# Kernel tuning notes

Hardware: AMD Instinct MI355X
Metric: run time of the kernel (lower is better)

Reference implementation:

```python
import jax, jax.numpy as jnp
import numpy as np

B, S, D, H = 2, 2048, 1024, 16
DEPTH = D // H


def setup_inputs() -> dict:
    key = jax.random.key(0)
    ks = jax.random.split(key, 12)
    sc = 1.0 / np.sqrt(D)
    n = lambda k, shp, s=sc: jax.random.normal(k, shp, dtype=jnp.float32) * s
    return {
        "q": jax.random.normal(ks[0], (B, S, D), dtype=jnp.float32),
        "k": jax.random.normal(ks[1], (B, S, D), dtype=jnp.float32),
        "v": jax.random.normal(ks[2], (B, S, D), dtype=jnp.float32),
        # key-padding mask: 1 = masked, 0 = keep (added to logits * -1e9)
        "mask": (jax.random.uniform(ks[3], (B, 1, 1, S)) < 0.1).astype(jnp.float32),
        "wq_w": n(ks[4], (D, D)), "wq_b": jnp.zeros((D,), jnp.float32),
        "wk_w": n(ks[5], (D, D)), "wk_b": jnp.zeros((D,), jnp.float32),
        "wv_w": n(ks[6], (D, D)), "wv_b": jnp.zeros((D,), jnp.float32),
        "dense_w": n(ks[7], (D, D)), "dense_b": jnp.zeros((D,), jnp.float32),
    }


def _split_heads(x, b, s):
    # [B, S, D] -> [B, H, S, depth]
    return x.reshape(b, s, H, DEPTH).transpose(0, 2, 1, 3)


def reference(q, k, v, mask, wq_w, wq_b, wk_w, wk_b, wv_w, wv_b, dense_w, dense_b):
    b, sq, _ = q.shape
    sk = k.shape[1]
    qh = _split_heads(q @ wq_w.T + wq_b, b, sq)
    kh = _split_heads(k @ wk_w.T + wk_b, b, sk)
    vh = _split_heads(v @ wv_w.T + wv_b, b, sk)
    scale = 1.0 / jnp.sqrt(jnp.float32(DEPTH))
    logits = jnp.einsum('bhqd,bhkd->bhqk', qh, kh) * scale  # [B,H,Sq,Sk]
    logits = logits + mask * (-1e9)
    attn = jax.nn.softmax(logits, axis=-1)
    ctx = jnp.einsum('bhqk,bhkd->bhqd', attn, vh)
    ctx = ctx.transpose(0, 2, 1, 3).reshape(b, sq, D)  # concat heads
    out = ctx @ dense_w.T + dense_b
    return out, attn
```

## Files before the change

kernel.cpp:

```cpp
#include <hip/hip_runtime.h>

#define BB 2
#define SS 2048
#define DD 1024
#define HH 16
#define DEPTH 64
#define MTOT (BB*SS)
#define QW 8
#define QBLK (QW*16)
#define NT (SS/64)
#define NPROJ ((size_t)BB*HH*SS*DEPTH)
#define WSZ   ((size_t)DD*DD)

using f16 = _Float16;
typedef _Float16 f16x8 __attribute__((ext_vector_type(8)));
typedef _Float16 f16x4 __attribute__((ext_vector_type(4)));
typedef float f32x4 __attribute__((ext_vector_type(4)));

#define GLOAD16(g, l) __builtin_amdgcn_global_load_lds(                      \
    (__attribute__((address_space(1))) const void*)(g),                      \
    (__attribute__((address_space(3))) void*)(l), 16, 0, 0)

__global__ __launch_bounds__(256) void cvt_kernel(
    const float* __restrict__ q, const float* __restrict__ k, const float* __restrict__ v,
    const float* __restrict__ w0, const float* __restrict__ w1, const float* __restrict__ w2,
    f16* __restrict__ qf, f16* __restrict__ kf, f16* __restrict__ vf,
    f16* __restrict__ wq, f16* __restrict__ wk, f16* __restrict__ wv)
{
    const int z = blockIdx.y;
    const float* s = z==0?q : z==1?k : z==2?v : z==3?w0 : z==4?w1 : w2;
    f16*        d = z==0?qf: z==1?kf: z==2?vf: z==3?wq: z==4?wk: wv;
    const size_t n = (z < 3) ? NPROJ : WSZ;
    for (size_t i = ((size_t)blockIdx.x * 256 + threadIdx.x) * 8; i < n;
         i += (size_t)gridDim.x * 256 * 8) {
        f32x4 a = *(const f32x4*)(s + i);
        f32x4 b = *(const f32x4*)(s + i + 4);
        f16x8 o = {(f16)a[0], (f16)a[1], (f16)a[2], (f16)a[3],
                   (f16)b[0], (f16)b[1], (f16)b[2], (f16)b[3]};
        *(f16x8*)(d + i) = o;
    }
}

__global__ __launch_bounds__(256) void proj_kernel(
    const f16* __restrict__ qf, const f16* __restrict__ kf, const f16* __restrict__ vf,
    const f16* __restrict__ wqw, const f16* __restrict__ wkw, const f16* __restrict__ wvw,
    const float* __restrict__ bq, const float* __restrict__ bk, const float* __restrict__ bv,
    f16* __restrict__ qh, f16* __restrict__ kh, f16* __restrict__ vt)
{
    const int mode = blockIdx.z;
    const f16* A    = mode==0 ? qf  : mode==1 ? kf  : vf;
    const f16* Bw   = mode==0 ? wqw : mode==1 ? wkw : wvw;
    const float* bias = mode==0 ? bq : mode==1 ? bk : bv;

    __shared__ f16 As[128*64];
    __shared__ f16 Bs[128*64];

    const int tid = threadIdx.x, wave = tid >> 6, lane = tid & 63;
    const int m0 = blockIdx.y * 128, n0 = blockIdx.x * 128;
    const int wm = (wave >> 1) * 64, wn = (wave & 1) * 64;
    const int lrow = lane & 15, g = lane >> 4;
    const int sw = lrow & 7;
    const int srow = tid >> 3;
    const int schk = (tid & 7) ^ (srow & 7);

    f32x4 acc[4][4] = {};

    for (int kk = 0; kk < DD; kk += 64) {
        #pragma unroll
        for (int i = 0; i < 4; ++i) {
            GLOAD16(A  + (size_t)(m0 + i*32 + srow) * DD + kk + schk * 8,
                    &As[i*2048 + wave*512]);
            GLOAD16(Bw + (size_t)(n0 + i*32 + srow) * DD + kk + schk * 8,
                    &Bs[i*2048 + wave*512]);
        }
        __syncthreads();
        for (int kf2 = 0; kf2 < 2; ++kf2) {
            f16x8 a[4], bf[4];
            for (int i = 0; i < 4; ++i)
                a[i]  = *(const f16x8*)&As[(wm + i*16 + lrow)*64 + ((kf2*4 + g) ^ sw)*8];
            for (int i = 0; i < 4; ++i)
                bf[i] = *(const f16x8*)&Bs[(wn + i*16 + lrow)*64 + ((kf2*4 + g) ^ sw)*8];
            for (int mi = 0; mi < 4; ++mi)
                for (int ni = 0; ni < 4; ++ni)
                    acc[mi][ni] = __builtin_amdgcn_mfma_f32_16x16x32_f16(a[mi], bf[ni], acc[mi][ni], 0, 0, 0);
        }
        __syncthreads();
    }

    const int rbase = g * 4;
    if (mode == 2) {
        for (int ni = 0; ni < 4; ++ni) {
            int n = n0 + wn + ni * 16 + lrow;
            float bval = bias[n];
            int hh = n >> 6, dep = n & 63;
            for (int mi = 0; mi < 4; ++mi) {
                int m = m0 + wm + mi * 16 + rbase;
                int bb = m >> 11, s = m & 2047;
                f16x4 pk = {(f16)(acc[mi][ni][0] + bval), (f16)(acc[mi][ni][1] + bval),
                            (f16)(acc[mi][ni][2] + bval), (f16)(acc[mi][ni][3] + bval)};
                *(f16x4*)&vt[((size_t)(bb * HH + hh) * DEPTH + dep) * SS + s] = pk;
            }
        }
    } else {
        f16* dst = (mode == 0) ? qh : kh;
        for (int ni = 0; ni < 4; ++ni) {
            int n = n0 + wn + ni * 16 + lrow;
            float bval = bias[n];
            int hh = n >> 6, dep = n & 63;
            for (int mi = 0; mi < 4; ++mi)
                for (int j = 0; j < 4; ++j) {
                    int m = m0 + wm + mi * 16 + rbase + j;
                    int bb = m >> 11, s = m & 2047;
                    dst[((size_t)(bb * HH + hh) * SS + s) * DEPTH + dep] = (f16)(acc[mi][ni][j] + bval);
                }
        }
    }
}

__global__ __launch_bounds__(512) void attn_kernel(
    const f16* __restrict__ qh, const f16* __restrict__ kh, const f16* __restrict__ vt,
    const float* __restrict__ mask, float* __restrict__ attn_out, f16* __restrict__ ctx)
{
    __shared__ float mlds[SS];
    __shared__ f16 Ks[2][64*64];
    __shared__ f16 Vs[2][64*64];
    __shared__ f16 Pl[QW][16][72];

    const int tid = threadIdx.x, wave = tid >> 6, lane = tid & 63;
    const int L = blockIdx.x;
    const int xcd = L & 7, iw = L >> 3;
    const int bh = xcd * 4 + (iw >> 4);
    const int qb = iw & 15;
    const int b = bh >> 4, h = bh & 15;
    const int q0 = qb * QBLK;
    const int lrow = lane & 15, g = lane >> 4;
    const int rbase = g * 4;
    const int sw = lrow & 7;
    const int srow = tid >> 3;
    const int schk = (tid & 7) ^ (srow & 7);

    const f16* Qbase = qh + (size_t)bh * SS * DEPTH;
    const f16* Kb = kh + (size_t)bh * SS * DEPTH;
    const f16* Vb = vt + (size_t)bh * DEPTH * SS;

    for (int i = tid; i < SS; i += 512) mlds[i] = mask[b * SS + i] * -1e9f;

    f16x8 aq[2];
    for (int kf2 = 0; kf2 < 2; ++kf2)
        aq[kf2] = *(const f16x8*)(Qbase + (size_t)(q0 + wave*16 + lrow) * DEPTH + kf2*32 + g*8);

    float s_l[4] = {0.f, 0.f, 0.f, 0.f};
    GLOAD16(Kb + (size_t)(0*64 + srow) * DEPTH + schk * 8, &Ks[0][wave * 512]);
    __syncthreads();
    for (int kt = 0; kt < NT; ++kt) {
        const int cur = kt & 1;
        if (kt + 1 < NT)
            GLOAD16(Kb + (size_t)((kt+1)*64 + srow) * DEPTH + schk * 8, &Ks[cur ^ 1][wave * 512]);
        for (int nf = 0; nf < 4; ++nf) {
            f32x4 a4 = {};
            for (int kf2 = 0; kf2 < 2; ++kf2) {
                f16x8 bf = *(const f16x8*)&Ks[cur][(nf*16 + lrow)*64 + ((kf2*4 + g) ^ sw)*8];
                a4 = __builtin_amdgcn_mfma_f32_16x16x32_f16(aq[kf2], bf, a4, 0, 0, 0);
            }
            float mb = mlds[kt*64 + nf*16 + lrow];
            for (int j = 0; j < 4; ++j) s_l[j] += __expf(a4[j] * 0.125f + mb);
        }
        __syncthreads();
    }
    for (int j = 0; j < 4; ++j) {
        float s = s_l[j];
        for (int off = 1; off < 16; off <<= 1) s += __shfl_xor(s, off);
        s_l[j] = 1.0f / s;
    }

    f32x4 cacc[4] = {};
    float* arow = attn_out + ((size_t)bh * SS + q0 + wave * 16) * SS;
    GLOAD16(Kb + (size_t)(0*64 + srow) * DEPTH + schk * 8, &Ks[0][wave * 512]);
    GLOAD16(Vb + (size_t)srow * SS + 0*64 + schk * 8,      &Vs[0][wave * 512]);
    __syncthreads();
    for (int kt = 0; kt < NT; ++kt) {
        const int cur = kt & 1;
        if (kt + 1 < NT) {
            GLOAD16(Kb + (size_t)((kt+1)*64 + srow) * DEPTH + schk * 8, &Ks[cur ^ 1][wave * 512]);
            GLOAD16(Vb + (size_t)srow * SS + (kt+1)*64 + schk * 8,      &Vs[cur ^ 1][wave * 512]);
        }
        for (int nf = 0; nf < 4; ++nf) {
            f32x4 a4 = {};
            for (int kf2 = 0; kf2 < 2; ++kf2) {
                f16x8 bf = *(const f16x8*)&Ks[cur][(nf*16 + lrow)*64 + ((kf2*4 + g) ^ sw)*8];
                a4 = __builtin_amdgcn_mfma_f32_16x16x32_f16(aq[kf2], bf, a4, 0, 0, 0);
            }
            float mb = mlds[kt*64 + nf*16 + lrow];
            for (int j = 0; j < 4; ++j) {
                float p = __expf(a4[j] * 0.125f + mb) * s_l[j];
                Pl[wave][rbase + j][nf*16 + lrow] = (f16)p;
            }
        }
        for (int i = 0; i < 4; ++i) {
            int r = i * 4 + g;
            f16x4 pv4 = *(const f16x4*)&Pl[wave][r][lrow * 4];
            f32x4 o = {(float)pv4[0], (float)pv4[1], (float)pv4[2], (float)pv4[3]};
            __builtin_nontemporal_store(o, (f32x4*)&arow[(size_t)r * SS + kt*64 + lrow*4]);
        }
        for (int kf2 = 0; kf2 < 2; ++kf2) {
            f16x8 pa = *(const f16x8*)&Pl[wave][lrow][kf2*32 + g*8];
            for (int nf = 0; nf < 4; ++nf) {
                f16x8 bv = *(const f16x8*)&Vs[cur][(nf*16 + lrow)*64 + ((kf2*4 + g) ^ sw)*8];
                cacc[nf] = __builtin_amdgcn_mfma_f32_16x16x32_f16(pa, bv, cacc[nf], 0, 0, 0);
            }
        }
        __syncthreads();
    }
    for (int nf = 0; nf < 4; ++nf)
        for (int j = 0; j < 4; ++j) {
            int qrow = q0 + wave * 16 + rbase + j;
            ctx[((size_t)(b * SS + qrow) * HH + h) * DEPTH + nf*16 + lrow] = (f16)cacc[nf][j];
        }
}

__global__ __launch_bounds__(256) void dense_kernel(
    const f16* __restrict__ ctx, const float* __restrict__ W,
    const float* __restrict__ bias, float* __restrict__ out)
{
    __shared__ f16 As[128][72];
    __shared__ f16 Bs[128][72];

    const int tid = threadIdx.x;
    const int wave = tid >> 6, lane = tid & 63;
    const int m0 = blockIdx.y * 128, n0 = blockIdx.x * 128;
    const int wm = (wave >> 1) * 64, wn = (wave & 1) * 64;
    const int lrow = lane & 15, lko = (lane >> 4) * 8;

    f32x4 acc[4][4] = {};

    for (int kk = 0; kk < DD; kk += 64) {
        __syncthreads();
        for (int i = 0; i < 4; ++i) {
            int c = tid + i * 256;
            int r = c >> 3, c8 = c & 7;
            *(f16x8*)&As[r][c8 * 8] = *(const f16x8*)(ctx + (size_t)(m0 + r) * DD + kk + c8 * 8);
        }
        for (int i = 0; i < 8; ++i) {
            int c = tid + i * 256;
            int r = c >> 4, c4 = c & 15;
            f32x4 bv4 = *(const f32x4*)(W + (size_t)(n0 + r) * DD + kk + c4 * 4);
            *(f16x4*)&Bs[r][c4 * 4] = (f16x4){(f16)bv4[0], (f16)bv4[1], (f16)bv4[2], (f16)bv4[3]};
        }
        __syncthreads();
        for (int kf = 0; kf < 2; ++kf) {
            f16x8 a[4], bf[4];
            for (int i = 0; i < 4; ++i) a[i]  = *(const f16x8*)&As[wm + i*16 + lrow][kf*32 + lko];
            for (int i = 0; i < 4; ++i) bf[i] = *(const f16x8*)&Bs[wn + i*16 + lrow][kf*32 + lko];
            for (int mi = 0; mi < 4; ++mi)
                for (int ni = 0; ni < 4; ++ni)
                    acc[mi][ni] = __builtin_amdgcn_mfma_f32_16x16x32_f16(a[mi], bf[ni], acc[mi][ni], 0, 0, 0);
        }
    }

    const int rbase = (lane >> 4) * 4;
    for (int ni = 0; ni < 4; ++ni) {
        int n = n0 + wn + ni * 16 + lrow;
        float bval = bias[n];
        for (int mi = 0; mi < 4; ++mi)
            for (int j = 0; j < 4; ++j) {
                int m = m0 + wm + mi * 16 + rbase + j;
                out[(size_t)m * DD + n] = acc[mi][ni][j] + bval;
            }
    }
}

extern "C" void kernel_launch(void* const* d_in, const int* in_sizes, int n_in,
                              void* d_out, int out_size, void* d_ws, size_t ws_size,
                              hipStream_t stream) {
    const float* q       = (const float*)d_in[0];
    const float* k       = (const float*)d_in[1];
    const float* v       = (const float*)d_in[2];
    const float* mask    = (const float*)d_in[3];
    const float* wq_w    = (const float*)d_in[4];
    const float* wq_b    = (const float*)d_in[5];
    const float* wk_w    = (const float*)d_in[6];
    const float* wk_b    = (const float*)d_in[7];
    const float* wv_w    = (const float*)d_in[8];
    const float* wv_b    = (const float*)d_in[9];
    const float* dense_w = (const float*)d_in[10];
    const float* dense_b = (const float*)d_in[11];

    float* out  = (float*)d_out;
    float* attn = out + (size_t)MTOT * DD;

    f16* qh  = (f16*)d_ws;
    f16* kh  = qh + NPROJ;
    f16* vt  = kh + NPROJ;
    f16* ctx = vt + NPROJ;

    f16* sc   = (f16*)attn;
    f16* qf   = sc;
    f16* kf   = sc + NPROJ;
    f16* vf   = sc + 2*NPROJ;
    f16* wq16 = sc + 3*NPROJ;
    f16* wk16 = wq16 + WSZ;
    f16* wv16 = wk16 + WSZ;

    cvt_kernel<<<dim3(1024, 6), 256, 0, stream>>>(q, k, v, wq_w, wk_w, wv_w,
                                                  qf, kf, vf, wq16, wk16, wv16);
    proj_kernel<<<dim3(8, 32, 3), 256, 0, stream>>>(qf, kf, vf, wq16, wk16, wv16,
                                                    wq_b, wk_b, wv_b, qh, kh, vt);
    attn_kernel<<<dim3(512), 512, 0, stream>>>(qh, kh, vt, mask, attn, ctx);
    dense_kernel<<<dim3(8, 32), 256, 0, stream>>>(ctx, dense_w, dense_b, out);
}
```

Before: 235.3 us.

## Transpose QK MFMA output so each lane owns one query row

Swaps the MFMA operands so each lane holds four consecutive key columns of a single query row. The row-sum reduction then needs two cross-group shuffles instead of per-row 16-lane butterflies, and the mask is read as a vector. Attention probabilities are stored straight from registers as fp32 vector stores, with no round trip through LDS, and the stored values are no longer truncated to fp16. The exponent is computed with native exp2 using a pre-folded log2(e) scale, at the cost of a different store access pattern and some rounding difference.

```diff
diff --git a/kernel.cpp b/kernel.cpp
--- a/kernel.cpp
+++ b/kernel.cpp
@@ -16,6 +16,9 @@
 typedef _Float16 f16x8 __attribute__((ext_vector_type(8)));
 typedef _Float16 f16x4 __attribute__((ext_vector_type(4)));
 typedef float f32x4 __attribute__((ext_vector_type(4)));
+
+#define LOG2E 1.44269504088896f
+#define SC2   (0.125f * LOG2E)
 
 #define GLOAD16(g, l) __builtin_amdgcn_global_load_lds(                      \
     (__attribute__((address_space(1))) const void*)(g),                      \
@@ -143,13 +146,13 @@
     const f16* Kb = kh + (size_t)bh * SS * DEPTH;
     const f16* Vb = vt + (size_t)bh * DEPTH * SS;
 
-    for (int i = tid; i < SS; i += 512) mlds[i] = mask[b * SS + i] * -1e9f;
+    for (int i = tid; i < SS; i += 512) mlds[i] = mask[b * SS + i] * (-1e9f * LOG2E);
 
     f16x8 aq[2];
     for (int kf2 = 0; kf2 < 2; ++kf2)
         aq[kf2] = *(const f16x8*)(Qbase + (size_t)(q0 + wave*16 + lrow) * DEPTH + kf2*32 + g*8);
 
-    float s_l[4] = {0.f, 0.f, 0.f, 0.f};
+    float s_l = 0.f;
     GLOAD16(Kb + (size_t)(0*64 + srow) * DEPTH + schk * 8, &Ks[0][wave * 512]);
     __syncthreads();
     for (int kt = 0; kt < NT; ++kt) {
@@ -160,21 +163,20 @@
             f32x4 a4 = {};
             for (int kf2 = 0; kf2 < 2; ++kf2) {
                 f16x8 bf = *(const f16x8*)&Ks[cur][(nf*16 + lrow)*64 + ((kf2*4 + g) ^ sw)*8];
-                a4 = __builtin_amdgcn_mfma_f32_16x16x32_f16(aq[kf2], bf, a4, 0, 0, 0);
-            }
-            float mb = mlds[kt*64 + nf*16 + lrow];
-            for (int j = 0; j < 4; ++j) s_l[j] += __expf(a4[j] * 0.125f + mb);
-        }
-        __syncthreads();
-    }
-    for (int j = 0; j < 4; ++j) {
-        float s = s_l[j];
-        for (int off = 1; off < 16; off <<= 1) s += __shfl_xor(s, off);
-        s_l[j] = 1.0f / s;
-    }
+                a4 = __builtin_amdgcn_mfma_f32_16x16x32_f16(bf, aq[kf2], a4, 0, 0, 0);
+            }
+            f32x4 mb4 = *(const f32x4*)&mlds[kt*64 + nf*16 + g*4];
+            for (int j = 0; j < 4; ++j)
+                s_l += __builtin_amdgcn_exp2f(a4[j] * SC2 + mb4[j]);
+        }
+        __syncthreads();
+    }
+    s_l += __shfl_xor(s_l, 16);
+    s_l += __shfl_xor(s_l, 32);
+    const float s_inv = 1.0f / s_l;
 
     f32x4 cacc[4] = {};
-    float* arow = attn_out + ((size_t)bh * SS + q0 + wave * 16) * SS;
+    float* arow = attn_out + ((size_t)bh * SS + q0 + wave * 16 + lrow) * SS;
     GLOAD16(Kb + (size_t)(0*64 + srow) * DEPTH + schk * 8, &Ks[0][wave * 512]);
     GLOAD16(Vb + (size_t)srow * SS + 0*64 + schk * 8,      &Vs[0][wave * 512]);
     __syncthreads();
@@ -188,19 +190,15 @@
             f32x4 a4 = {};
             for (int kf2 = 0; kf2 < 2; ++kf2) {
                 f16x8 bf = *(const f16x8*)&Ks[cur][(nf*16 + lrow)*64 + ((kf2*4 + g) ^ sw)*8];
-                a4 = __builtin_amdgcn_mfma_f32_16x16x32_f16(aq[kf2], bf, a4, 0, 0, 0);
-            }
-            float mb = mlds[kt*64 + nf*16 + lrow];
-            for (int j = 0; j < 4; ++j) {
-                float p = __expf(a4[j] * 0.125f + mb) * s_l[j];
-                Pl[wave][rbase + j][nf*16 + lrow] = (f16)p;
-            }
-        }
-        for (int i = 0; i < 4; ++i) {
-            int r = i * 4 + g;
-            f16x4 pv4 = *(const f16x4*)&Pl[wave][r][lrow * 4];
-            f32x4 o = {(float)pv4[0], (float)pv4[1], (float)pv4[2], (float)pv4[3]};
-            __builtin_nontemporal_store(o, (f32x4*)&arow[(size_t)r * SS + kt*64 + lrow*4]);
+                a4 = __builtin_amdgcn_mfma_f32_16x16x32_f16(bf, aq[kf2], a4, 0, 0, 0);
+            }
+            f32x4 mb4 = *(const f32x4*)&mlds[kt*64 + nf*16 + g*4];
+            f32x4 p;
+            for (int j = 0; j < 4; ++j)
+                p[j] = __builtin_amdgcn_exp2f(a4[j] * SC2 + mb4[j]) * s_inv;
+            __builtin_nontemporal_store(p, (f32x4*)&arow[kt*64 + nf*16 + g*4]);
+            f16x4 p4 = {(f16)p[0], (f16)p[1], (f16)p[2], (f16)p[3]};
+            *(f16x4*)&Pl[wave][lrow][nf*16 + g*4] = p4;
         }
         for (int kf2 = 0; kf2 < 2; ++kf2) {
             f16x8 pa = *(const f16x8*)&Pl[wave][lrow][kf2*32 + g*8];
```

Result: slower. 299.0 us (+27.0%).

## Pre-convert dense weights to fp16, use async LDS loads in dense GEMM, exp2 softmax

Applied to the files above, without the earlier changes.

A new kernel converts the dense weight to fp16 into the no-longer-needed qh workspace. The dense GEMM then loads both operands with global_load_lds straight into an XOR-swizzled unpadded LDS layout, instead of register-staged loads with in-loop fp32 to fp16 conversion. Separately, the softmax exp is rewritten as exp2 with log2e folded into the scale and mask, which saves a multiply per element. The cost is one extra kernel launch and an extra pass over the weight matrix.

```diff
diff --git a/kernel.cpp b/kernel.cpp
--- a/kernel.cpp
+++ b/kernel.cpp
@@ -17,6 +17,9 @@
 typedef _Float16 f16x4 __attribute__((ext_vector_type(4)));
 typedef float f32x4 __attribute__((ext_vector_type(4)));
 
+#define LOG2E 1.44269504088896f
+#define SC2   (0.125f * LOG2E)
+
 #define GLOAD16(g, l) __builtin_amdgcn_global_load_lds(                      \
     (__attribute__((address_space(1))) const void*)(g),                      \
     (__attribute__((address_space(3))) void*)(l), 16, 0, 0)
@@ -33,6 +36,19 @@
     const size_t n = (z < 3) ? NPROJ : WSZ;
     for (size_t i = ((size_t)blockIdx.x * 256 + threadIdx.x) * 8; i < n;
          i += (size_t)gridDim.x * 256 * 8) {
+        f32x4 a = *(const f32x4*)(s + i);
+        f32x4 b = *(const f32x4*)(s + i + 4);
+        f16x8 o = {(f16)a[0], (f16)a[1], (f16)a[2], (f16)a[3],
+                   (f16)b[0], (f16)b[1], (f16)b[2], (f16)b[3]};
+        *(f16x8*)(d + i) = o;
+    }
+}
+
+__global__ __launch_bounds__(256) void cvt2_kernel(
+    const float* __restrict__ s, f16* __restrict__ d)
+{
+    size_t i = ((size_t)blockIdx.x * 256 + threadIdx.x) * 8;
+    if (i < WSZ) {
         f32x4 a = *(const f32x4*)(s + i);
         f32x4 b = *(const f32x4*)(s + i + 4);
         f16x8 o = {(f16)a[0], (f16)a[1], (f16)a[2], (f16)a[3],
@@ -143,7 +159,7 @@
     const f16* Kb = kh + (size_t)bh * SS * DEPTH;
     const f16* Vb = vt + (size_t)bh * DEPTH * SS;
 
-    for (int i = tid; i < SS; i += 512) mlds[i] = mask[b * SS + i] * -1e9f;
+    for (int i = tid; i < SS; i += 512) mlds[i] = mask[b * SS + i] * (-1e9f * LOG2E);
 
     f16x8 aq[2];
     for (int kf2 = 0; kf2 < 2; ++kf2)
@@ -163,7 +179,8 @@
                 a4 = __builtin_amdgcn_mfma_f32_16x16x32_f16(aq[kf2], bf, a4, 0, 0, 0);
             }
             float mb = mlds[kt*64 + nf*16 + lrow];
-            for (int j = 0; j < 4; ++j) s_l[j] += __expf(a4[j] * 0.125f + mb);
+            for (int j = 0; j < 4; ++j)
+                s_l[j] += __builtin_amdgcn_exp2f(a4[j] * SC2 + mb);
         }
         __syncthreads();
     }
@@ -192,7 +209,7 @@
             }
             float mb = mlds[kt*64 + nf*16 + lrow];
             for (int j = 0; j < 4; ++j) {
-                float p = __expf(a4[j] * 0.125f + mb) * s_l[j];
+                float p = __builtin_amdgcn_exp2f(a4[j] * SC2 + mb) * s_l[j];
                 Pl[wave][rbase + j][nf*16 + lrow] = (f16)p;
             }
         }
@@ -219,45 +236,45 @@
 }
 
 __global__ __launch_bounds__(256) void dense_kernel(
-    const f16* __restrict__ ctx, const float* __restrict__ W,
+    const f16* __restrict__ ctx, const f16* __restrict__ W16,
     const float* __restrict__ bias, float* __restrict__ out)
 {
-    __shared__ f16 As[128][72];
-    __shared__ f16 Bs[128][72];
-
-    const int tid = threadIdx.x;
-    const int wave = tid >> 6, lane = tid & 63;
+    __shared__ f16 As[128*64];
+    __shared__ f16 Bs[128*64];
+
+    const int tid = threadIdx.x, wave = tid >> 6, lane = tid & 63;
     const int m0 = blockIdx.y * 128, n0 = blockIdx.x * 128;
     const int wm = (wave >> 1) * 64, wn = (wave & 1) * 64;
-    const int lrow = lane & 15, lko = (lane >> 4) * 8;
+    const int lrow = lane & 15, g = lane >> 4;
+    const int sw = lrow & 7;
+    const int srow = tid >> 3;
+    const int schk = (tid & 7) ^ (srow & 7);
 
     f32x4 acc[4][4] = {};
 
     for (int kk = 0; kk < DD; kk += 64) {
-        __syncthreads();
+        #pragma unroll
         for (int i = 0; i < 4; ++i) {
-            int c = tid + i * 256;
-            int r = c >> 3, c8 = c & 7;
-            *(f16x8*)&As[r][c8 * 8] = *(const f16x8*)(ctx + (size_t)(m0 + r) * DD + kk + c8 * 8);
-        }
-        for (int i = 0; i < 8; ++i) {
-            int c = tid + i * 256;
-            int r = c >> 4, c4 = c & 15;
-            f32x4 bv4 = *(const f32x4*)(W + (size_t)(n0 + r) * DD + kk + c4 * 4);
-            *(f16x4*)&Bs[r][c4 * 4] = (f16x4){(f16)bv4[0], (f16)bv4[1], (f16)bv4[2], (f16)bv4[3]};
-        }
-        __syncthreads();
-        for (int kf = 0; kf < 2; ++kf) {
+            GLOAD16(ctx + (size_t)(m0 + i*32 + srow) * DD + kk + schk * 8,
+                    &As[i*2048 + wave*512]);
+            GLOAD16(W16 + (size_t)(n0 + i*32 + srow) * DD + kk + schk * 8,
+                    &Bs[i*2048 + wave*512]);
+        }
+        __syncthreads();
+        for (int kf2 = 0; kf2 < 2; ++kf2) {
             f16x8 a[4], bf[4];
-            for (int i = 0; i < 4; ++i) a[i]  = *(const f16x8*)&As[wm + i*16 + lrow][kf*32 + lko];
-            for (int i = 0; i < 4; ++i) bf[i] = *(const f16x8*)&Bs[wn + i*16 + lrow][kf*32 + lko];
+            for (int i = 0; i < 4; ++i)
+                a[i]  = *(const f16x8*)&As[(wm + i*16 + lrow)*64 + ((kf2*4 + g) ^ sw)*8];
+            for (int i = 0; i < 4; ++i)
+                bf[i] = *(const f16x8*)&Bs[(wn + i*16 + lrow)*64 + ((kf2*4 + g) ^ sw)*8];
             for (int mi = 0; mi < 4; ++mi)
                 for (int ni = 0; ni < 4; ++ni)
                     acc[mi][ni] = __builtin_amdgcn_mfma_f32_16x16x32_f16(a[mi], bf[ni], acc[mi][ni], 0, 0, 0);
         }
-    }
-
-    const int rbase = (lane >> 4) * 4;
+        __syncthreads();
+    }
+
+    const int rbase = g * 4;
     for (int ni = 0; ni < 4; ++ni) {
         int n = n0 + wn + ni * 16 + lrow;
         float bval = bias[n];
@@ -301,10 +318,13 @@
     f16* wk16 = wq16 + WSZ;
     f16* wv16 = wk16 + WSZ;
 
+    f16* dw16 = qh;
+
     cvt_kernel<<<dim3(1024, 6), 256, 0, stream>>>(q, k, v, wq_w, wk_w, wv_w,
                                                   qf, kf, vf, wq16, wk16, wv16);
     proj_kernel<<<dim3(8, 32, 3), 256, 0, stream>>>(qf, kf, vf, wq16, wk16, wv16,
                                                     wq_b, wk_b, wv_b, qh, kh, vt);
     attn_kernel<<<dim3(512), 512, 0, stream>>>(qh, kh, vt, mask, attn, ctx);
-    dense_kernel<<<dim3(8, 32), 256, 0, stream>>>(ctx, dense_w, dense_b, out);
-}
+    cvt2_kernel<<<dim3(512), 256, 0, stream>>>(dense_w, dw16);
+    dense_kernel<<<dim3(8, 32), 256, 0, stream>>>(ctx, dw16, dense_b, out);
+}
```

After: 235.6 us. About the same (+0.1%).
